# Kernel tuning notes

Measured on AMD Instinct MI355X. Metric: run time of the kernel, lower is better.

## Reference

```python
import jax, jax.numpy as jnp
import numpy as np
from jax import lax

IN_CH = 256
UP = 8
DN = ('NCHW', 'OIHW', 'NCHW')


def setup_inputs() -> dict:
    key = jax.random.key(0)
    ks = jax.random.split(key, 6)
    B, H, W = 8, 96, 96
    flow_lr = jax.random.normal(ks[0], (B, 2, H, W), dtype=jnp.float32)
    feat = jax.random.normal(ks[1], (B, IN_CH, H, W), dtype=jnp.float32)
    w1 = jax.random.normal(ks[2], (IN_CH, IN_CH, 3, 3), dtype=jnp.float32) * 0.02
    b1 = jnp.zeros((IN_CH,), dtype=jnp.float32)
    w2 = jax.random.normal(ks[3], (UP * UP * 9, IN_CH, 1, 1), dtype=jnp.float32) * 0.02
    b2 = jnp.zeros((UP * UP * 9,), dtype=jnp.float32)
    return {"flow_lr": flow_lr, "feat": feat, "w1": w1, "b1": b1, "w2": w2, "b2": b2}


def reference(flow_lr, feat, w1, b1, w2, b2):
    B, _, H, W = flow_lr.shape
    up = UP
    # mask head: 3x3 conv + relu + 1x1 conv
    x = lax.conv_general_dilated(feat, w1, (1, 1), 'SAME', dimension_numbers=DN)
    x = jax.nn.relu(x + b1[None, :, None, None])
    mask = lax.conv_general_dilated(x, w2, (1, 1), 'SAME', dimension_numbers=DN)
    mask = mask + b2[None, :, None, None]
    # channel dim 9*up*up splits as (9, up, up), matching torch .view(B,1,9,up,up,H,W)
    mask = mask.reshape(B, 9, up, up, H, W)
    mask = jax.nn.softmax(mask, axis=1)
    # unfold(flow_lr, 3, padding=1): 9 zero-padded 3x3 shifts, row-major (kh, kw)
    pad = jnp.pad(flow_lr, ((0, 0), (0, 0), (1, 1), (1, 1)))
    flow_unf = jnp.stack(
        [pad[:, :, i:i + H, j:j + W] for i in range(3) for j in range(3)], axis=2
    )  # (B, 2, 9, H, W)
    # convex combination over the 9 neighbors
    up_flow = jnp.einsum('bkpqhw,bckhw->bcpqhw', mask, flow_unf)  # (B,2,up,up,H,W)
    # pixel-shuffle: (B,2,p,q,H,W) -> (B,2,H,p,W,q) -> (B,2,H*up,W*up)
    up_flow = up_flow.transpose(0, 1, 4, 2, 5, 3).reshape(B, 2, H * up, W * up)
    return up_flow * up
```

## Files before the change

### kernel.cpp

```cpp
#include <hip/hip_runtime.h>
#include <hip/hip_bf16.h>
#include <stdint.h>

typedef unsigned short u16;
typedef __bf16 bf16x8 __attribute__((ext_vector_type(8)));
typedef float f32x4 __attribute__((ext_vector_type(4)));

#define MFMA16(a, b, c) __builtin_amdgcn_mfma_f32_16x16x32_bf16((a), (b), (c), 0, 0, 0)

#define GLOAD16(g, l)                                                        \
  __builtin_amdgcn_global_load_lds(                                          \
      (const __attribute__((address_space(1))) void*)(g),                    \
      (__attribute__((address_space(3))) void*)(l), 16, 0, 0)

static __device__ __forceinline__ u16 f2bf(float f) {
  union { float f; uint32_t u; } v;
  v.f = f;
  uint32_t u = v.u;
  return (u16)((u + 0x7FFFu + ((u >> 16) & 1u)) >> 16);
}

#define FEATT_ELEMS (8u * 98u * 98u * 256u)
#define W1T_OFF     FEATT_ELEMS
#define W1T_ELEMS   (256u * 2304u)
#define W2B_OFF     (W1T_OFF + W1T_ELEMS)
#define W2B_ELEMS   (576u * 256u)
#define X_OFF       (W2B_OFF + W2B_ELEMS)

__global__ __launch_bounds__(256) void prep_featT(const float* __restrict__ feat,
                                                  u16* __restrict__ featT) {
  const int pt = blockIdx.x, ct = blockIdx.y, b = blockIdx.z;
  const int p0 = pt * 64, c0 = ct * 64;
  __shared__ float tile[64][65];
  const int t = threadIdx.x;
  const int pj = t & 63, ci0 = t >> 6;
#pragma unroll
  for (int r = 0; r < 16; ++r) {
    int ci = r * 4 + ci0;
    tile[ci][pj] = feat[(b * 256 + c0 + ci) * 9216 + p0 + pj];
  }
  __syncthreads();
  const int pl = t >> 2, cc0 = (t & 3) * 16;
  const int pix = p0 + pl;
  const int h = pix / 96, w = pix % 96;
  uint32_t u[8];
#pragma unroll
  for (int i = 0; i < 8; ++i) {
    u16 lo = f2bf(tile[cc0 + 2 * i][pl]);
    u16 hi = f2bf(tile[cc0 + 2 * i + 1][pl]);
    u[i] = (uint32_t)lo | ((uint32_t)hi << 16);
  }
  uint4* dst = (uint4*)(featT + (size_t)((b * 98 + h + 1) * 98 + (w + 1)) * 256 + c0 + cc0);
  dst[0] = make_uint4(u[0], u[1], u[2], u[3]);
  dst[1] = make_uint4(u[4], u[5], u[6], u[7]);
}

__global__ __launch_bounds__(256) void prep_w(const float* __restrict__ w1,
                                              const float* __restrict__ w2,
                                              u16* __restrict__ w1t,
                                              u16* __restrict__ w2b) {
  int i = blockIdx.x * 256 + threadIdx.x;
  if (i < 589824) {
    int oc = i / 2304, r = i % 2304;
    int tap = r >> 8, cin = r & 255;
    w1t[i] = f2bf(w1[(oc * 256 + cin) * 9 + tap]);
  } else {
    int j = i - 589824;
    if (j < 147456) w2b[j] = f2bf(w2[j]);
  }
}

__global__ __launch_bounds__(256, 2) void gemm1(const u16* __restrict__ featT,
                                                const u16* __restrict__ w1t,
                                                const float* __restrict__ b1,
                                                u16* __restrict__ xout) {
  __shared__ __align__(16) u16 sA[2][128 * 64];
  __shared__ __align__(16) u16 sB[2][128 * 64];
  __shared__ float sb1[128];

  const int t = threadIdx.x;
  const int wave = t >> 6, lane = t & 63;
  const int nt = blockIdx.x & 1, mt = blockIdx.x >> 1;
  const int b = mt / 72;
  const int ip0 = (mt % 72) * 128;
  const int oc0 = nt * 128;

  if (t < 128) sb1[t] = b1[oc0 + t];

  const u16* aBase[4];
  const u16* bBase[4];
#pragma unroll
  for (int r = 0; r < 4; ++r) {
    int row = (wave * 4 + r) * 8 + (lane >> 3);
    int chunk = (lane & 7) ^ (row & 7);
    int ip = ip0 + row;
    int h = ip / 96, w = ip % 96;
    aBase[r] = featT + (size_t)((b * 98 + h + 1) * 98 + (w + 1)) * 256 + chunk * 8;
    bBase[r] = w1t + (size_t)(oc0 + row) * 2304 + chunk * 8;
  }

  auto stage = [&](int kt, int bufi) {
    int tap = kt >> 2;
    int dh = tap / 3 - 1, dw = tap % 3 - 1;
    int aoff = (dh * 98 + dw) * 256 + (kt & 3) * 64;
    int boff = kt * 64;
#pragma unroll
    for (int r = 0; r < 4; ++r) {
      GLOAD16(aBase[r] + aoff, &sA[bufi][(wave * 4 + r) * 512]);
      GLOAD16(bBase[r] + boff, &sB[bufi][(wave * 4 + r) * 512]);
    }
  };

  const int wm = wave >> 1, wn = wave & 1;
  int aoffs[4][2], boffs[4][2];
#pragma unroll
  for (int m = 0; m < 4; ++m) {
#pragma unroll
    for (int ki = 0; ki < 2; ++ki) {
      int kc = ki * 4 + (lane >> 4);
      int rowa = wm * 64 + m * 16 + (lane & 15);
      aoffs[m][ki] = rowa * 64 + ((kc ^ (rowa & 7)) * 8);
      int rowb = wn * 64 + m * 16 + (lane & 15);
      boffs[m][ki] = rowb * 64 + ((kc ^ (rowb & 7)) * 8);
    }
  }

  f32x4 acc[4][4];
#pragma unroll
  for (int m = 0; m < 4; ++m)
#pragma unroll
    for (int n = 0; n < 4; ++n) acc[m][n] = f32x4{0.f, 0.f, 0.f, 0.f};

  stage(0, 0);
  int buf = 0;
  for (int kt = 0; kt < 36; ++kt) {
    __syncthreads();
    if (kt < 35) stage(kt + 1, buf ^ 1);
#pragma unroll
    for (int ki = 0; ki < 2; ++ki) {
      bf16x8 av[4], bv[4];
#pragma unroll
      for (int m = 0; m < 4; ++m) av[m] = *(const bf16x8*)&sA[buf][aoffs[m][ki]];
#pragma unroll
      for (int n = 0; n < 4; ++n) bv[n] = *(const bf16x8*)&sB[buf][boffs[n][ki]];
#pragma unroll
      for (int m = 0; m < 4; ++m)
#pragma unroll
        for (int n = 0; n < 4; ++n) acc[m][n] = MFMA16(av[m], bv[n], acc[m][n]);
    }
    buf ^= 1;
  }

  const int pix0g = mt * 128;
#pragma unroll
  for (int m = 0; m < 4; ++m) {
    int pixl = wm * 64 + m * 16 + ((lane >> 4) << 2);
#pragma unroll
    for (int n = 0; n < 4; ++n) {
      int oc = wn * 64 + n * 16 + (lane & 15);
      float bias = sb1[oc];
      f32x4 v = acc[m][n];
#pragma unroll
      for (int j = 0; j < 4; ++j) {
        float val = v[j] + bias;
        val = val > 0.f ? val : 0.f;
        xout[(size_t)(pix0g + pixl + j) * 256 + oc0 + oc] = f2bf(val);
      }
    }
  }
}

__global__ __launch_bounds__(512, 1) void gemm2(const u16* __restrict__ xws,
                                                const u16* __restrict__ w2b,
                                                const float* __restrict__ b2,
                                                const float* __restrict__ flow,
                                                float* __restrict__ out) {
  __shared__ __align__(16) u16 sX[128 * 256];
  __shared__ __align__(16) u16 sB2[2][144 * 64];
  __shared__ float sFlow[2][9][128];
  __shared__ float sb2[576];

  const int t = threadIdx.x;
  const int wave = t >> 6, lane = t & 63;
  const int mt = blockIdx.x;
  const int b = mt / 72;
  const int ip0 = (mt % 72) * 128;

#pragma unroll
  for (int r = 0; r < 8; ++r) {
    int wr = r * 8 + wave;
    int pix = wr * 2 + (lane >> 5);
    int cpos = lane & 31;
    const u16* src = xws + (size_t)(mt * 128 + pix) * 256 + ((cpos ^ (pix & 7)) * 8);
    GLOAD16(src, &sX[wr * 512]);
  }
  for (int i = t; i < 2304; i += 512) {
    int c = i / 1152, rem = i % 1152;
    int k = rem >> 7, p = rem & 127;
    int ip = ip0 + p;
    int h = ip / 96, w = ip % 96;
    int hh = h + k / 3 - 1, ww = w + k % 3 - 1;
    float v = 0.f;
    if (hh >= 0 && hh < 96 && ww >= 0 && ww < 96)
      v = flow[((b * 2 + c) * 96 + hh) * 96 + ww];
    sFlow[c][k][p] = v;
  }
  for (int i = t; i < 576; i += 512) sb2[i] = b2[i];

  auto stageB = [&](int step, int bufi) {
    int chunkI = step >> 2, ks = step & 3;
#pragma unroll
    for (int r = 0; r < 3; ++r) {
      int wr = r * 8 + wave;
      if (wr < 18) {
        int row = wr * 8 + (lane >> 3);
        int c = (row >> 4) * 64 + chunkI * 16 + (row & 15);
        const u16* src = w2b + (size_t)c * 256 + ks * 64 + (((lane & 7) ^ (row & 7)) * 8);
        GLOAD16(src, &sB2[bufi][wr * 512]);
      }
    }
  };

  stageB(0, 0);
  int buf = 0;
  f32x4 acc[9];
#pragma unroll
  for (int nf = 0; nf < 9; ++nf) acc[nf] = f32x4{0.f, 0.f, 0.f, 0.f};
  const int pixl = wave * 16 + (lane & 15);

  for (int step = 0; step < 16; ++step) {
    __syncthreads();
    if (step < 15) stageB(step + 1, buf ^ 1);
    int ks = step & 3;
#pragma unroll
    for (int ki = 0; ki < 2; ++ki) {
      int c32 = ks * 8 + ki * 4 + (lane >> 4);
      bf16x8 a = *(const bf16x8*)&sX[pixl * 256 + ((c32 ^ (pixl & 7)) * 8)];
      int kc = ki * 4 + (lane >> 4);
#pragma unroll
      for (int nf = 0; nf < 9; ++nf) {
        int row = nf * 16 + (lane & 15);
        bf16x8 bv = *(const bf16x8*)&sB2[buf][row * 64 + ((kc ^ (row & 7)) * 8)];
        acc[nf] = MFMA16(a, bv, acc[nf]);
      }
    }
    if (ks == 3) {
      int chunkI = step >> 2;
      int pql = lane & 15;
      int p = chunkI * 2 + (pql >> 3), q = pql & 7;
#pragma unroll
      for (int j = 0; j < 4; ++j) {
        int pe = wave * 16 + ((lane >> 4) << 2) + j;
        float v[9], mx = -3.0e38f;
#pragma unroll
        for (int nf = 0; nf < 9; ++nf) {
          v[nf] = acc[nf][j] + sb2[nf * 64 + chunkI * 16 + pql];
          mx = fmaxf(mx, v[nf]);
        }
        float s = 0.f, fx = 0.f, fy = 0.f;
#pragma unroll
        for (int nf = 0; nf < 9; ++nf) {
          float e = __expf(v[nf] - mx);
          s += e;
          fx += e * sFlow[0][nf][pe];
          fy += e * sFlow[1][nf][pe];
        }
        float sc = 8.0f / s;
        int ip = ip0 + pe;
        int h = ip / 96, w = ip % 96;
        size_t o0 = ((size_t)(b * 2 + 0) * 768 + h * 8 + p) * 768 + w * 8 + q;
        size_t o1 = ((size_t)(b * 2 + 1) * 768 + h * 8 + p) * 768 + w * 8 + q;
        out[o0] = fx * sc;
        out[o1] = fy * sc;
      }
#pragma unroll
      for (int nf = 0; nf < 9; ++nf) acc[nf] = f32x4{0.f, 0.f, 0.f, 0.f};
    }
    buf ^= 1;
  }
}

extern "C" void kernel_launch(void* const* d_in, const int* in_sizes, int n_in,
                              void* d_out, int out_size, void* d_ws, size_t ws_size,
                              hipStream_t stream) {
  const float* flow = (const float*)d_in[0];
  const float* feat = (const float*)d_in[1];
  const float* w1 = (const float*)d_in[2];
  const float* b1 = (const float*)d_in[3];
  const float* w2 = (const float*)d_in[4];
  const float* b2 = (const float*)d_in[5];
  float* out = (float*)d_out;
  u16* ws = (u16*)d_ws;
  u16* featT = ws;
  u16* w1t = ws + W1T_OFF;
  u16* w2b = ws + W2B_OFF;
  u16* xws = ws + X_OFF;

  hipMemsetAsync(featT, 0, (size_t)FEATT_ELEMS * 2, stream);
  prep_featT<<<dim3(144, 4, 8), 256, 0, stream>>>(feat, featT);
  prep_w<<<2880, 256, 0, stream>>>(w1, w2, w1t, w2b);
  gemm1<<<1152, 256, 0, stream>>>(featT, w1t, b1, xws);
  gemm2<<<576, 512, 0, stream>>>(xws, w2b, b2, flow, out);
}
```

Measured before the change: 218.8 us.

## Zero only halo, widen gemm1 tile to full N, cache A in registers in gemm2

```diff
diff --git a/kernel.cpp b/kernel.cpp
--- a/kernel.cpp
+++ b/kernel.cpp
@@ -26,6 +26,20 @@
 #define W2B_OFF     (W1T_OFF + W1T_ELEMS)
 #define W2B_ELEMS   (576u * 256u)
 #define X_OFF       (W2B_OFF + W2B_ELEMS)
+
+__global__ __launch_bounds__(256) void halo_zero(u16* __restrict__ featT) {
+  int tid = blockIdx.x * 256 + threadIdx.x;
+  int b = tid / (388 * 32);
+  int rem = tid % (388 * 32);
+  int pos = rem >> 5, v = rem & 31;
+  int h, w;
+  if (pos < 98) { h = 0; w = pos; }
+  else if (pos < 196) { h = 97; w = pos - 98; }
+  else if (pos < 292) { h = pos - 196 + 1; w = 0; }
+  else { h = pos - 292 + 1; w = 97; }
+  uint4* dst = (uint4*)(featT + (size_t)((b * 98 + h) * 98 + w) * 256 + v * 8);
+  *dst = make_uint4(0, 0, 0, 0);
+}
 
 __global__ __launch_bounds__(256) void prep_featT(const float* __restrict__ feat,
                                                   u16* __restrict__ featT) {
@@ -70,48 +84,40 @@
   }
 }
 
-__global__ __launch_bounds__(256, 2) void gemm1(const u16* __restrict__ featT,
+__global__ __launch_bounds__(512, 4) void gemm1(const u16* __restrict__ featT,
                                                 const u16* __restrict__ w1t,
                                                 const float* __restrict__ b1,
                                                 u16* __restrict__ xout) {
-  __shared__ __align__(16) u16 sA[2][128 * 64];
-  __shared__ __align__(16) u16 sB[2][128 * 64];
-  __shared__ float sb1[128];
+  __shared__ __align__(16) u16 sA[128 * 64];
+  __shared__ __align__(16) u16 sB[256 * 64];
+  __shared__ float sb1[256];
 
   const int t = threadIdx.x;
   const int wave = t >> 6, lane = t & 63;
-  const int nt = blockIdx.x & 1, mt = blockIdx.x >> 1;
+  const int mt = blockIdx.x;
   const int b = mt / 72;
   const int ip0 = (mt % 72) * 128;
-  const int oc0 = nt * 128;
-
-  if (t < 128) sb1[t] = b1[oc0 + t];
-
-  const u16* aBase[4];
+
+  if (t < 256) sb1[t] = b1[t];
+
+  const u16* aBase[2];
   const u16* bBase[4];
 #pragma unroll
-  for (int r = 0; r < 4; ++r) {
-    int row = (wave * 4 + r) * 8 + (lane >> 3);
+  for (int r = 0; r < 2; ++r) {
+    int row = r * 64 + wave * 8 + (lane >> 3);
     int chunk = (lane & 7) ^ (row & 7);
     int ip = ip0 + row;
     int h = ip / 96, w = ip % 96;
     aBase[r] = featT + (size_t)((b * 98 + h + 1) * 98 + (w + 1)) * 256 + chunk * 8;
-    bBase[r] = w1t + (size_t)(oc0 + row) * 2304 + chunk * 8;
-  }
-
-  auto stage = [&](int kt, int bufi) {
-    int tap = kt >> 2;
-    int dh = tap / 3 - 1, dw = tap % 3 - 1;
-    int aoff = (dh * 98 + dw) * 256 + (kt & 3) * 64;
-    int boff = kt * 64;
-#pragma unroll
-    for (int r = 0; r < 4; ++r) {
-      GLOAD16(aBase[r] + aoff, &sA[bufi][(wave * 4 + r) * 512]);
-      GLOAD16(bBase[r] + boff, &sB[bufi][(wave * 4 + r) * 512]);
-    }
-  };
-
-  const int wm = wave >> 1, wn = wave & 1;
+  }
+#pragma unroll
+  for (int r = 0; r < 4; ++r) {
+    int row = wave * 32 + r * 8 + (lane >> 3);
+    int chunk = (lane & 7) ^ (row & 7);
+    bBase[r] = w1t + (size_t)row * 2304 + chunk * 8;
+  }
+
+  const int wm = wave >> 2, wn = wave & 3;
   int aoffs[4][2], boffs[4][2];
 #pragma unroll
   for (int m = 0; m < 4; ++m) {
@@ -131,24 +137,29 @@
 #pragma unroll
     for (int n = 0; n < 4; ++n) acc[m][n] = f32x4{0.f, 0.f, 0.f, 0.f};
 
-  stage(0, 0);
-  int buf = 0;
   for (int kt = 0; kt < 36; ++kt) {
+    int tap = kt >> 2;
+    int dh = tap / 3 - 1, dw = tap % 3 - 1;
+    int aoff = (dh * 98 + dw) * 256 + (kt & 3) * 64;
+    int boff = kt * 64;
+#pragma unroll
+    for (int r = 0; r < 2; ++r) GLOAD16(aBase[r] + aoff, &sA[(r * 64 + wave * 8) * 64]);
+#pragma unroll
+    for (int r = 0; r < 4; ++r) GLOAD16(bBase[r] + boff, &sB[(wave * 32 + r * 8) * 64]);
     __syncthreads();
-    if (kt < 35) stage(kt + 1, buf ^ 1);
 #pragma unroll
     for (int ki = 0; ki < 2; ++ki) {
       bf16x8 av[4], bv[4];
 #pragma unroll
-      for (int m = 0; m < 4; ++m) av[m] = *(const bf16x8*)&sA[buf][aoffs[m][ki]];
-#pragma unroll
-      for (int n = 0; n < 4; ++n) bv[n] = *(const bf16x8*)&sB[buf][boffs[n][ki]];
+      for (int m = 0; m < 4; ++m) av[m] = *(const bf16x8*)&sA[aoffs[m][ki]];
+#pragma unroll
+      for (int n = 0; n < 4; ++n) bv[n] = *(const bf16x8*)&sB[boffs[n][ki]];
 #pragma unroll
       for (int m = 0; m < 4; ++m)
 #pragma unroll
         for (int n = 0; n < 4; ++n) acc[m][n] = MFMA16(av[m], bv[n], acc[m][n]);
     }
-    buf ^= 1;
+    __syncthreads();
   }
 
   const int pix0g = mt * 128;
@@ -164,19 +175,18 @@
       for (int j = 0; j < 4; ++j) {
         float val = v[j] + bias;
         val = val > 0.f ? val : 0.f;
-        xout[(size_t)(pix0g + pixl + j) * 256 + oc0 + oc] = f2bf(val);
+        xout[(size_t)(pix0g + pixl + j) * 256 + oc] = f2bf(val);
       }
     }
   }
 }
 
-__global__ __launch_bounds__(512, 1) void gemm2(const u16* __restrict__ xws,
+__global__ __launch_bounds__(512, 4) void gemm2(const u16* __restrict__ xws,
                                                 const u16* __restrict__ w2b,
                                                 const float* __restrict__ b2,
                                                 const float* __restrict__ flow,
                                                 float* __restrict__ out) {
-  __shared__ __align__(16) u16 sX[128 * 256];
-  __shared__ __align__(16) u16 sB2[2][144 * 64];
+  __shared__ __align__(16) u16 smem0[128 * 256];
   __shared__ float sFlow[2][9][128];
   __shared__ float sb2[576];
 
@@ -192,7 +202,7 @@
     int pix = wr * 2 + (lane >> 5);
     int cpos = lane & 31;
     const u16* src = xws + (size_t)(mt * 128 + pix) * 256 + ((cpos ^ (pix & 7)) * 8);
-    GLOAD16(src, &sX[wr * 512]);
+    GLOAD16(src, &smem0[wr * 512]);
   }
   for (int i = t; i < 2304; i += 512) {
     int c = i / 1152, rem = i % 1152;
@@ -206,6 +216,16 @@
     sFlow[c][k][p] = v;
   }
   for (int i = t; i < 576; i += 512) sb2[i] = b2[i];
+  __syncthreads();
+
+  const int pixl = wave * 16 + (lane & 15);
+  bf16x8 areg[8];
+#pragma unroll
+  for (int s = 0; s < 8; ++s) {
+    int kc = s * 4 + (lane >> 4);
+    areg[s] = *(const bf16x8*)&smem0[pixl * 256 + ((kc ^ (pixl & 7)) * 8)];
+  }
+  __syncthreads();
 
   auto stageB = [&](int step, int bufi) {
     int chunkI = step >> 2, ks = step & 3;
@@ -216,31 +236,30 @@
         int row = wr * 8 + (lane >> 3);
         int c = (row >> 4) * 64 + chunkI * 16 + (row & 15);
         const u16* src = w2b + (size_t)c * 256 + ks * 64 + (((lane & 7) ^ (row & 7)) * 8);
-        GLOAD16(src, &sB2[bufi][wr * 512]);
+        GLOAD16(src, &smem0[bufi * 9216 + wr * 512]);
       }
     }
   };
 
   stageB(0, 0);
-  int buf = 0;
   f32x4 acc[9];
 #pragma unroll
   for (int nf = 0; nf < 9; ++nf) acc[nf] = f32x4{0.f, 0.f, 0.f, 0.f};
-  const int pixl = wave * 16 + (lane & 15);
-
+
+#pragma unroll
   for (int step = 0; step < 16; ++step) {
     __syncthreads();
-    if (step < 15) stageB(step + 1, buf ^ 1);
-    int ks = step & 3;
+    if (step < 15) stageB(step + 1, (step & 1) ^ 1);
+    const int buf = step & 1;
+    const int ks = step & 3;
 #pragma unroll
     for (int ki = 0; ki < 2; ++ki) {
-      int c32 = ks * 8 + ki * 4 + (lane >> 4);
-      bf16x8 a = *(const bf16x8*)&sX[pixl * 256 + ((c32 ^ (pixl & 7)) * 8)];
       int kc = ki * 4 + (lane >> 4);
+      bf16x8 a = areg[ks * 2 + ki];
 #pragma unroll
       for (int nf = 0; nf < 9; ++nf) {
         int row = nf * 16 + (lane & 15);
-        bf16x8 bv = *(const bf16x8*)&sB2[buf][row * 64 + ((kc ^ (row & 7)) * 8)];
+        bf16x8 bv = *(const bf16x8*)&smem0[buf * 9216 + row * 64 + ((kc ^ (row & 7)) * 8)];
         acc[nf] = MFMA16(a, bv, acc[nf]);
       }
     }
@@ -276,7 +295,6 @@
 #pragma unroll
       for (int nf = 0; nf < 9; ++nf) acc[nf] = f32x4{0.f, 0.f, 0.f, 0.f};
     }
-    buf ^= 1;
   }
 }
 
@@ -296,9 +314,9 @@
   u16* w2b = ws + W2B_OFF;
   u16* xws = ws + X_OFF;
 
-  hipMemsetAsync(featT, 0, (size_t)FEATT_ELEMS * 2, stream);
+  halo_zero<<<388, 256, 0, stream>>>(featT);
   prep_featT<<<dim3(144, 4, 8), 256, 0, stream>>>(feat, featT);
   prep_w<<<2880, 256, 0, stream>>>(w1, w2, w1t, w2b);
-  gemm1<<<1152, 256, 0, stream>>>(featT, w1t, b1, xws);
+  gemm1<<<576, 512, 0, stream>>>(featT, w1t, b1, xws);
   gemm2<<<576, 512, 0, stream>>>(xws, w2b, b2, flow, out);
 }
```

New measurement: 231.9 us. 6.0% more time.
